# Kernel optimization log

Measured on AMD Instinct MI355X. Metric: run time of the kernel, lower is better.

The kernel has to match this reference:

```python
import jax, jax.numpy as jnp
import numpy as np

L = 16
B = 128
_PERM = np.array([0, 6, 2, 4, 3, 5, 1, 7])  # stabilizer swap permutation


def _swap_stabilizers(t):
    # t: (b, L, L, L, 8, 2, 2, 2). Torch does permute(0,4,3,2,1) on (N,8,2,2,2)
    # rows, i.e. reverse the trailing 4 dims, reshape back, then permute dim -4.
    shape = t.shape
    t = jnp.transpose(t, (0, 1, 2, 3, 7, 6, 5, 4)).reshape(shape)
    return t[:, :, :, :, _PERM]


def _surface_to_flags(surf):
    # surf: (..., L) int. flip, roll 1, cumsum, roll 1, parity.
    s = jnp.flip(surf, axis=-1)
    s = jnp.roll(s, 1, axis=-1)
    c = jnp.roll(jnp.cumsum(s, axis=-1), 1, axis=-1)
    return (c % 2) > 0


def _get_z_flag(syn_str, axis, shift, l):
    b = syn_str.shape[0]
    syn = syn_str.reshape(b, l, l, l)
    r = jnp.roll(syn, shift, axis=3 - axis)
    surf = jnp.sum(r, axis=1 + axis)  # (b, l, l)
    return _surface_to_flags(surf)


def _get_x_flag(syn_str, axis, shift, l):
    b = syn_str.shape[0]
    syn = syn_str.reshape(b, l, l, l)
    r = jnp.roll(syn, shift, axis=3 - axis)
    surf = jnp.sum(r, axis=(1 + axis, 1 + (1 + axis) % 3))  # (b, l)
    return _surface_to_flags(surf)


def _logic_action_average(probs, syndrome, axis, l):
    b = probs.shape[0]
    z_syn, x0, x1, x2 = jnp.split(syndrome, 4, axis=1)
    x_ch = (x0, x1, x2)[axis]

    # --- Z (dual lattice) update ---
    fz = _get_z_flag(z_syn, axis=axis, shift=0, l=l)  # (b, l, l)
    # torch: fz.unsqueeze(-1).repeat(1,1,1,l).permute(0,3,2,1)
    # => mask[b,i,j,k] = fz[b,k,j]
    mask_z = jnp.broadcast_to(jnp.transpose(fz, (0, 2, 1))[:, None], (b, l, l, l))
    cand = _swap_stabilizers(probs)
    cand = jnp.roll(cand, 1, axis=-3 + axis)  # roll one of the trailing 2-dims
    cand = _swap_stabilizers(cand)
    probs = jnp.where(mask_z[..., None, None, None, None], cand, probs)

    # --- X (primal lattice) update ---
    fx = _get_x_flag(x_ch, axis=axis, shift=1, l=l)  # (b, l)
    # torch: fx[...,None,None].repeat(1,1,l,l).permute(0,3,2,1)
    # => mask[b,i,j,k] = fx[b,k]
    mask_x = jnp.broadcast_to(fx[:, None, None, :], (b, l, l, l))
    rolled = jnp.roll(probs, 1, axis=-1 - axis)
    probs = jnp.where(mask_x[..., None, None, None, None], rolled, probs)
    return probs


def setup_inputs() -> dict:
    key = jax.random.key(0)
    k1, k2 = jax.random.split(key)
    x = jax.random.uniform(k1, (B, L, L, L, 8, 2, 2, 2), dtype=jnp.float32)
    syndrome = jax.random.randint(k2, (B, 4 * L ** 3), 0, 2, dtype=jnp.int32)
    return {"x": x, "syndrome": syndrome}


def reference(x, syndrome) -> jnp.ndarray:
    l = L
    for axis in range(3):
        x = _logic_action_average(x, syndrome, axis, l)
        x = jnp.transpose(x, (0, 2, 3, 1, 4, 5, 6, 7))
    return jnp.mean(x, axis=(1, 2, 3))  # (b, 8, 2, 2, 2)
```

## Files before the change

### kernel.cpp

```cpp
#include <hip/hip_runtime.h>
#include <stdint.h>

#define BATCH 128

#define OFF_FZ0 0
#define OFF_FZ1 (OFF_FZ0 + BATCH * 256)
#define OFF_FZ2 (OFF_FZ1 + BATCH * 256)
#define OFF_FX0 (OFF_FZ2 + BATCH * 256)
#define OFF_FX1 (OFF_FX0 + BATCH * 16)
#define OFF_FX2 (OFF_FX1 + BATCH * 16)

__device__ __forceinline__ int A_of(int o) {
    return ((o & 7) << 3) | (((o >> 3) & 1) << 2) | (((o >> 4) & 1) << 1) | ((o >> 5) & 1);
}
__device__ __forceinline__ int S_of(int o) {
    const unsigned P = (0u) | (6u << 3) | (2u << 6) | (4u << 9) | (3u << 12) |
                       (5u << 15) | (1u << 18) | (7u << 21);
    int s = (int)((P >> (3 * (o >> 3))) & 7u);
    return A_of((s << 3) | (o & 7));
}

__device__ __forceinline__ unsigned flag16(const unsigned char* r, int pos) {
    unsigned f;
    if (pos == 0) {
        f = 0;
#pragma unroll
        for (int w = 0; w < 16; ++w) f ^= r[w];
    } else {
        f = r[0];
        for (int w = 17 - pos; w <= 15; ++w) f ^= r[w];
    }
    return f & 1u;
}

__global__ __launch_bounds__(256) void k_flags(const int* __restrict__ syn,
                                               unsigned char* __restrict__ ws) {
    int b = blockIdx.x, job = blockIdx.y, t = threadIdx.x;
    int dhi = t >> 4, dlo = t & 15;
    const int* base = syn + (size_t)b * 16384;
    __shared__ unsigned char sp[256];
    __shared__ unsigned char g[16];
    unsigned p = 0;

    if (job == 0) {
        const int* z = base;
#pragma unroll
        for (int d1 = 0; d1 < 16; ++d1) p ^= (unsigned)z[d1 * 256 + t];
        sp[t] = p & 1;
        __syncthreads();
        ws[OFF_FZ0 + b * 256 + t] = (unsigned char)flag16(&sp[dhi * 16], dlo);
    } else if (job == 1) {
        const int* z = base;
#pragma unroll
        for (int d2 = 0; d2 < 16; ++d2) p ^= (unsigned)z[dhi * 256 + d2 * 16 + dlo];
        sp[t] = p & 1;
        __syncthreads();
        ws[OFF_FZ1 + b * 256 + t] = (unsigned char)flag16(&sp[dhi * 16], dlo);
    } else if (job == 2) {
        const int* z = base;
#pragma unroll
        for (int d3 = 0; d3 < 16; ++d3) p ^= (unsigned)z[dhi * 256 + dlo * 16 + d3];
        sp[t] = p & 1;
        __syncthreads();
        ws[OFF_FZ2 + b * 256 + t] = (unsigned char)flag16(&sp[dhi * 16], dlo);
    } else if (job == 3) {
        const int* x0 = base + 4096;
#pragma unroll
        for (int d1 = 0; d1 < 16; ++d1) p ^= (unsigned)x0[d1 * 256 + t];
        sp[t] = p & 1;
        __syncthreads();
        if (t < 16) {
            unsigned q = 0;
            for (int d2 = 0; d2 < 16; ++d2) q ^= sp[d2 * 16 + t];
            g[(t + 1) & 15] = q & 1;
        }
        __syncthreads();
        if (t < 16) ws[OFF_FX0 + b * 16 + t] = (unsigned char)flag16(g, t);
    } else if (job == 4) {
        const int* x1 = base + 8192;
#pragma unroll
        for (int d3 = 0; d3 < 16; ++d3) p ^= (unsigned)x1[dhi * 256 + dlo * 16 + d3];
        sp[t] = p & 1;
        __syncthreads();
        if (t < 16) {
            unsigned q = 0;
            for (int d2 = 0; d2 < 16; ++d2) q ^= sp[t * 16 + d2];
            g[t] = q & 1;
        }
        __syncthreads();
        if (t < 16) ws[OFF_FX1 + b * 16 + t] = (unsigned char)flag16(g, t);
    } else {
        const int* x2 = base + 12288;
#pragma unroll
        for (int d3 = 0; d3 < 16; ++d3) p ^= (unsigned)x2[dhi * 256 + dlo * 16 + d3];
        sp[t] = p & 1;
        __syncthreads();
        if (t < 16) {
            unsigned q = 0;
            for (int d1 = 0; d1 < 16; ++d1) q ^= sp[d1 * 16 + t];
            g[t] = q & 1;
        }
        __syncthreads();
        if (t < 16) ws[OFF_FX2 + b * 16 + t] = (unsigned char)flag16(g, t);
    }
}

typedef const __attribute__((address_space(1))) uint32_t glob_u32;
typedef __attribute__((address_space(3))) uint32_t lds_u32;
__device__ __forceinline__ void dma16(const float* g, float* l) {
    __builtin_amdgcn_global_load_lds((glob_u32*)g, (lds_u32*)l, 16, 0, 0);
}

__global__ __launch_bounds__(256) void k_main(const float* __restrict__ x,
                                              const unsigned char* __restrict__ ws,
                                              float* __restrict__ out) {
    __shared__ float buf[2][64 * 64];
    __shared__ unsigned char T[4096];
    __shared__ unsigned char fz0[256], fz1[256], fz2[256];
    __shared__ unsigned char fx0[16], fx1[16], fx2[16];
    __shared__ unsigned char mArr[256];
    __shared__ unsigned char Ctab[3][64];
    __shared__ float red[256];

    int b  = blockIdx.y;
    int i0 = blockIdx.x;
    int t  = threadIdx.x;
    int w  = t >> 6, v = t & 63;

    const float* xb = x + (((size_t)b * 4096 + (size_t)i0 * 256) << 6);

    {
        const float* gsrc = xb + ((w * 16) << 6) + (v << 2);
        float* ldst = &buf[0][(w * 16) << 6];
        dma16(gsrc,       ldst);
        dma16(gsrc + 256, ldst + 256);
        dma16(gsrc + 512, ldst + 512);
        dma16(gsrc + 768, ldst + 768);
    }

    fz0[t] = ws[OFF_FZ0 + b * 256 + t];
    fz1[t] = ws[OFF_FZ1 + b * 256 + t];
    fz2[t] = ws[OFF_FZ2 + b * 256 + t];
    if (t < 16) {
        fx0[t] = ws[OFF_FX0 + b * 16 + t];
        fx1[t] = ws[OFF_FX1 + b * 16 + t];
        fx2[t] = ws[OFF_FX2 + b * 16 + t];
    }
    if (t < 192) {
        int ax = t >> 6, o = t & 63;
        int bit = 4 >> ax;
        Ctab[ax][o] = (unsigned char)S_of(S_of(o) ^ bit);
    }
    __syncthreads();

    {
        int j0 = t >> 4, k0 = t & 15;
        unsigned m = (unsigned)fz0[k0 * 16 + j0]
                   | ((unsigned)fx0[k0] << 1)
                   | ((unsigned)fz1[i0 * 16 + k0] << 2)
                   | ((unsigned)fx1[i0] << 3)
                   | ((unsigned)fz2[j0 * 16 + i0] << 4)
                   | ((unsigned)fx2[j0] << 5);
        mArr[t] = (unsigned char)m;
    }
    for (int idx = t; idx < 4096; idx += 256) {
        int m = idx >> 6, vv = idx & 63;
        int src = vv;
        if (m & 32) src ^= 4;
        if (m & 16) src = Ctab[2][src];
        if (m & 8)  src ^= 2;
        if (m & 4)  src = Ctab[1][src];
        if (m & 2)  src ^= 1;
        if (m & 1)  src = Ctab[0][src];
        T[idx] = (unsigned char)src;
    }
    __syncthreads();

    float acc = 0.f;
    const unsigned char* Trow = T;
#pragma unroll
    for (int c = 0; c < 4; ++c) {
        if (c < 3) {
            const float* gsrc = xb + (((c + 1) * 64 + w * 16) << 6) + (v << 2);
            float* ldst = &buf[(c + 1) & 1][(w * 16) << 6];
            dma16(gsrc,       ldst);
            dma16(gsrc + 256, ldst + 256);
            dma16(gsrc + 512, ldst + 512);
            dma16(gsrc + 768, ldst + 768);
        }
        const float* bufw = &buf[c & 1][(w * 16) << 6];
        int sl_base = c * 64 + w * 16;
#pragma unroll
        for (int it = 0; it < 16; ++it) {
            int m   = mArr[sl_base + it];
            int src = Trow[(m << 6) | v];
            acc += bufw[(it << 6) | src];
        }
        __syncthreads();
    }

    red[t] = acc;
    __syncthreads();
    if (t < 64) {
        float s4 = red[t] + red[t + 64] + red[t + 128] + red[t + 192];
        atomicAdd(out + b * 64 + t, s4 * (1.0f / 4096.0f));
    }
}

extern "C" void kernel_launch(void* const* d_in, const int* in_sizes, int n_in,
                              void* d_out, int out_size, void* d_ws, size_t ws_size,
                              hipStream_t stream) {
    const float* x   = (const float*)d_in[0];
    const int*   syn = (const int*)d_in[1];
    float* out = (float*)d_out;
    unsigned char* ws = (unsigned char*)d_ws;

    hipMemsetAsync(d_out, 0, (size_t)out_size * sizeof(float), stream);
    k_flags<<<dim3(BATCH, 6), 256, 0, stream>>>(syn, ws);
    k_main<<<dim3(16, BATCH), 256, 0, stream>>>(x, ws, out);
}
```

Baseline: 199.3 us.

## Replace LDS double-buffered DMA staging with direct gathered global loads

Removes the global_load_lds double-buffered staging of x tiles into shared memory, and the per-chunk barriers that went with it. Each thread now reads its permuted element straight from global memory, with the index looked up through the T table and 64 sites per wave. This cuts 32 KB of LDS per block, which may raise occupancy, and drops the syncs. The cost is non-contiguous gathered global loads within 256-byte rows and less explicit prefetch overlap.

```diff
diff --git a/kernel.cpp b/kernel.cpp
--- a/kernel.cpp
+++ b/kernel.cpp
@@ -105,16 +105,9 @@
     }
 }
 
-typedef const __attribute__((address_space(1))) uint32_t glob_u32;
-typedef __attribute__((address_space(3))) uint32_t lds_u32;
-__device__ __forceinline__ void dma16(const float* g, float* l) {
-    __builtin_amdgcn_global_load_lds((glob_u32*)g, (lds_u32*)l, 16, 0, 0);
-}
-
 __global__ __launch_bounds__(256) void k_main(const float* __restrict__ x,
                                               const unsigned char* __restrict__ ws,
                                               float* __restrict__ out) {
-    __shared__ float buf[2][64 * 64];
     __shared__ unsigned char T[4096];
     __shared__ unsigned char fz0[256], fz1[256], fz2[256];
     __shared__ unsigned char fx0[16], fx1[16], fx2[16];
@@ -128,15 +121,6 @@
     int w  = t >> 6, v = t & 63;
 
     const float* xb = x + (((size_t)b * 4096 + (size_t)i0 * 256) << 6);
-
-    {
-        const float* gsrc = xb + ((w * 16) << 6) + (v << 2);
-        float* ldst = &buf[0][(w * 16) << 6];
-        dma16(gsrc,       ldst);
-        dma16(gsrc + 256, ldst + 256);
-        dma16(gsrc + 512, ldst + 512);
-        dma16(gsrc + 768, ldst + 768);
-    }
 
     fz0[t] = ws[OFF_FZ0 + b * 256 + t];
     fz1[t] = ws[OFF_FZ1 + b * 256 + t];
@@ -176,27 +160,14 @@
     }
     __syncthreads();
 
+    const unsigned char* Tv = T + v;
+    int sbase = w * 64;
     float acc = 0.f;
-    const unsigned char* Trow = T;
-#pragma unroll
-    for (int c = 0; c < 4; ++c) {
-        if (c < 3) {
-            const float* gsrc = xb + (((c + 1) * 64 + w * 16) << 6) + (v << 2);
-            float* ldst = &buf[(c + 1) & 1][(w * 16) << 6];
-            dma16(gsrc,       ldst);
-            dma16(gsrc + 256, ldst + 256);
-            dma16(gsrc + 512, ldst + 512);
-            dma16(gsrc + 768, ldst + 768);
-        }
-        const float* bufw = &buf[c & 1][(w * 16) << 6];
-        int sl_base = c * 64 + w * 16;
-#pragma unroll
-        for (int it = 0; it < 16; ++it) {
-            int m   = mArr[sl_base + it];
-            int src = Trow[(m << 6) | v];
-            acc += bufw[(it << 6) | src];
-        }
-        __syncthreads();
+#pragma unroll 16
+    for (int s = 0; s < 64; ++s) {
+        int m   = mArr[sbase + s];
+        int src = Tv[m << 6];
+        acc += xb[((sbase + s) << 6) | src];
     }
 
     red[t] = acc;
```

Result: no change. 200.6 us (+0.6%).
